# Kernel tuning notes

Hardware: AMD Instinct MI355X
Metric: run time of the kernel (lower is better)

## Reference

```python
import jax, jax.numpy as jnp
import numpy as np

# Grid constants derived from init kwargs: min_pt=0, max_pt=128, step=1, eps=1e-8
ORIGIN = -(1.0 + 1e-8)          # per-dim origin of control grid
STEP = 1.0
MAX_COORD = 130.0               # control_grid_size (132) - 2
PTS_N = 2_000_000
GRID = 132
CHANNELS = 1


def setup_inputs() -> dict:
    key = jax.random.key(0)
    k1, k2 = jax.random.split(key)
    # points in world coords, uniform over the interpolable domain
    pts = jax.random.uniform(k1, (PTS_N, 3), dtype=jnp.float32) * 128.0
    control_pts = jax.random.normal(k2, (CHANNELS, GRID, GRID, GRID), dtype=jnp.float32)
    return {"pts": pts, "control_pts": control_pts}


def _coefs(x):
    # Cardinal cubic B-spline basis (Irwin-Hall n=4), x in [0,1). [pts] -> [pts,4]
    omx = 1.0 - x
    c0 = omx ** 3
    c1 = 3.0 * (x - 2.0) * x ** 2 + 4.0
    c2 = -3.0 * omx ** 2 * (x + 1.0) + 4.0
    c3 = x ** 3
    return jnp.stack([c0, c1, c2, c3], axis=-1) / 6.0


def reference(pts, control_pts):
    padding_value = 0.0
    # to control-grid coordinates
    t = (pts - ORIGIN) / STEP                                   # [P,3]
    in_bounds = jnp.all(t >= 1.0, axis=-1) & jnp.all(t < MAX_COORD, axis=-1)  # [P]
    t = jnp.where(in_bounds[:, None], t, 1.0)
    ti = t.astype(jnp.int32)                                    # trunc == floor since t>=1
    frac = t - ti.astype(t.dtype)                               # [P,3]
    w = _coefs(frac.reshape(-1)).reshape(-1, 3, 4)              # [P,3,4]

    stencil = jnp.arange(-1, 3, dtype=jnp.int32)                # [-1,0,1,2]
    idx = ti[..., None] + stencil                               # [P,3,4]
    # gather the 4x4x4 control-point stencil per point: [C,P,4,4,4]
    cp = control_pts[:, idx[:, 0, :, None, None], idx[:, 1, None, :, None], idx[:, 2, None, None, :]]
    # tensor-product weighted sum
    vals = jnp.einsum('cpijk,pi,pj,pk->pc', cp, w[:, 0], w[:, 1], w[:, 2])  # [P,C]
    vals = jnp.where(in_bounds[:, None], vals, jnp.float32(padding_value))
    return vals
```

## Files before the change

### kernel.cpp

```cpp
#include <hip/hip_runtime.h>

#define GRID_DIM 132
#define SLAB (GRID_DIM * GRID_DIM)
#define NB 512
#define CHUNK 2048
#define KPT (CHUNK / 256)
#define REG 20
#define REG2 (REG * REG)
#define REG3 (REG * REG * REG)
#define STRIPE 8192

__device__ __forceinline__ void bspline_w(float x, float w[4]) {
    float omx = 1.0f - x;
    w[0] = omx * omx * omx * (1.0f / 6.0f);
    w[1] = (3.0f * (x - 2.0f) * x * x + 4.0f) * (1.0f / 6.0f);
    w[2] = (-3.0f * omx * omx * (x + 1.0f) + 4.0f) * (1.0f / 6.0f);
    w[3] = x * x * x * (1.0f / 6.0f);
}

__device__ __forceinline__ void load_pt(const float* __restrict__ pts, int i,
                                        float& tx, float& ty, float& tz, bool& inb) {
    tx = pts[3 * i + 0] + 1.0f;
    ty = pts[3 * i + 1] + 1.0f;
    tz = pts[3 * i + 2] + 1.0f;
    inb = (tx >= 1.0f) && (ty >= 1.0f) && (tz >= 1.0f) &&
          (tx < 130.0f) && (ty < 130.0f) && (tz < 130.0f);
    if (!inb) { tx = ty = tz = 1.0f; }
}

__device__ __forceinline__ int calc_bin(float tx, float ty, float tz) {
    int bx = min(7, ((int)tx - 1) >> 4);
    int by = min(7, ((int)ty - 1) >> 4);
    int bz = min(7, ((int)tz - 1) >> 4);
    return (bx << 6) | (by << 3) | bz;
}

__device__ __forceinline__ void local_stripe_scan(
    const unsigned* __restrict__ stot, int nstripe,
    unsigned* soff, unsigned* sc)
{
    int t = threadIdx.x;
    if (t < 256) sc[t] = (t < nstripe) ? stot[t] : 0u;
    __syncthreads();
    for (int off = 1; off < 256; off <<= 1) {
        unsigned v = (t >= off && t < 256) ? sc[t - off] : 0u;
        __syncthreads();
        if (t < 256) sc[t] += v;
        __syncthreads();
    }
    if (t < 256) soff[t] = (t == 0) ? 0u : sc[t - 1];
    __syncthreads();
}

__global__ __launch_bounds__(256) void hist512_kernel(
    const float* __restrict__ pts, int n, int nblk, unsigned* __restrict__ bh)
{
    __shared__ unsigned lh[NB];
    int tid = threadIdx.x, blk = blockIdx.x;
    int c0 = blk * CHUNK;
    for (int b = tid; b < NB; b += 256) lh[b] = 0u;
    __syncthreads();
#pragma unroll
    for (int k = 0; k < KPT; ++k) {
        int i = c0 + tid + k * 256;
        if (i < n) {
            float tx, ty, tz; bool inb;
            load_pt(pts, i, tx, ty, tz, inb);
            atomicAdd(&lh[calc_bin(tx, ty, tz)], 1u);
        }
    }
    __syncthreads();
    for (int b = tid; b < NB; b += 256) bh[b * nblk + blk] = lh[b];
}

__global__ __launch_bounds__(256) void scan_l1_kernel(
    const unsigned* __restrict__ bh, unsigned* __restrict__ seg,
    unsigned* __restrict__ stot, int TOT)
{
    __shared__ unsigned sc[256];
    int t = threadIdx.x;
    int base_idx = blockIdx.x * STRIPE + t * 32;
    unsigned local[32];
    unsigned s = 0;
#pragma unroll
    for (int j = 0; j < 32; ++j) {
        int idx = base_idx + j;
        unsigned v = (idx < TOT) ? bh[idx] : 0u;
        local[j] = v; s += v;
    }
    sc[t] = s;
    __syncthreads();
    for (int off = 1; off < 256; off <<= 1) {
        unsigned v = (t >= off) ? sc[t - off] : 0u;
        __syncthreads();
        sc[t] += v;
        __syncthreads();
    }
    unsigned run = (t == 0) ? 0u : sc[t - 1];
#pragma unroll
    for (int j = 0; j < 32; ++j) {
        int idx = base_idx + j;
        if (idx < TOT) seg[idx] = run;
        run += local[j];
    }
    if (t == 255) stot[blockIdx.x] = sc[255];
}

__global__ __launch_bounds__(256) void partition_kernel(
    const float* __restrict__ pts, int n, int nblk,
    const unsigned* __restrict__ seg, const unsigned* __restrict__ stot,
    int nstripe, float4* __restrict__ sorted, unsigned* __restrict__ inv)
{
    __shared__ unsigned lcur[NB];
    __shared__ unsigned sc[256], soff[256];

    local_stripe_scan(stot, nstripe, soff, sc);

    int bid = blockIdx.x;
    int q = nblk >> 3, r = nblk & 7;
    int xcd = bid & 7, pos = bid >> 3;
    int blk = (xcd < r ? xcd * (q + 1) : r * (q + 1) + (xcd - r) * q) + pos;

    int tid = threadIdx.x;
    int c0 = blk * CHUNK;

    for (int b = tid; b < NB; b += 256) {
        int idx = b * nblk + blk;
        lcur[b] = seg[idx] + soff[idx >> 13];
    }
    __syncthreads();

#pragma unroll
    for (int k = 0; k < KPT; ++k) {
        int i = c0 + tid + k * 256;
        if (i < n) {
            float tx, ty, tz; bool inb;
            load_pt(pts, i, tx, ty, tz, inb);
            int bin = calc_bin(tx, ty, tz);
            unsigned g = atomicAdd(&lcur[bin], 1u);
            unsigned tag = (unsigned)i | (inb ? 0u : 0x80000000u);
            sorted[g] = make_float4(tx, ty, tz, __uint_as_float(tag));
            inv[i] = g;
        }
    }
}

__global__ __launch_bounds__(512) void eval_kernel(
    const float4* __restrict__ sorted, const float* __restrict__ cp,
    const unsigned* __restrict__ seg, const unsigned* __restrict__ stot,
    int nstripe, float* __restrict__ val_s, int n, int nblk)
{
    __shared__ float region[REG3];
    __shared__ unsigned sc[256], soff[256];

    local_stripe_scan(stot, nstripe, soff, sc);

    int bid = blockIdx.x;
    int bin = (bid & 7) * 64 + (bid >> 3);
    int x0 = (bin >> 6) << 4, y0 = ((bin >> 3) & 7) << 4, z0 = (bin & 7) << 4;

    const float* src = cp + (size_t)x0 * SLAB + y0 * GRID_DIM + z0;
    for (int v = threadIdx.x; v < REG3; v += 512) {
        int gx = v / REG2;
        int rr = v - gx * REG2;
        int gy = rr / REG;
        int gz = rr - gy * REG;
        region[v] = src[gx * SLAB + gy * GRID_DIM + gz];
    }
    __syncthreads();

    int i0 = bin * nblk;
    unsigned s = seg[i0] + soff[i0 >> 13];
    unsigned e;
    if (bin == NB - 1) e = (unsigned)n;
    else { int i1 = (bin + 1) * nblk; e = seg[i1] + soff[i1 >> 13]; }

    for (unsigned i = s + threadIdx.x; i < e; i += 512) {
        float4 p = sorted[i];
        unsigned tag = __float_as_uint(p.w);
        int ix = (int)p.x, iy = (int)p.y, iz = (int)p.z;
        float wx[4], wy[4], wz[4];
        bspline_w(p.x - (float)ix, wx);
        bspline_w(p.y - (float)iy, wy);
        bspline_w(p.z - (float)iz, wz);
        int lx = ix - 1 - x0, ly = iy - 1 - y0, lz = iz - 1 - z0;
        const float* rb = region + (lx * REG + ly) * REG + lz;
        float acc = 0.0f;
#pragma unroll
        for (int a = 0; a < 4; ++a) {
            float accy = 0.0f;
#pragma unroll
            for (int b = 0; b < 4; ++b) {
                const float* row = rb + (a * REG + b) * REG;
                float sz = fmaf(row[0], wz[0], fmaf(row[1], wz[1],
                           fmaf(row[2], wz[2], row[3] * wz[3])));
                accy = fmaf(wy[b], sz, accy);
            }
            acc = fmaf(wx[a], accy, acc);
        }
        val_s[i] = (tag >> 31) ? 0.0f : acc;
    }
}

__global__ __launch_bounds__(256) void unscatter_kernel(
    const float* __restrict__ val_s, const unsigned* __restrict__ inv,
    float* __restrict__ out, int n)
{
    int g = blockIdx.x * blockDim.x + threadIdx.x;
    int base = g * 4;
    if (base + 3 < n) {
        uint4 iv = ((const uint4*)inv)[g];
        float4 o;
        o.x = val_s[iv.x]; o.y = val_s[iv.y]; o.z = val_s[iv.z]; o.w = val_s[iv.w];
        ((float4*)out)[g] = o;
    } else if (base < n) {
        for (int k = base; k < n; ++k) out[k] = val_s[inv[k]];
    }
}

__global__ __launch_bounds__(256) void eval_unsorted_kernel(
    const float* __restrict__ pts, const float* __restrict__ cp,
    float* __restrict__ out, int n)
{
    int i = blockIdx.x * blockDim.x + threadIdx.x;
    if (i >= n) return;
    float tx, ty, tz; bool inb;
    load_pt(pts, i, tx, ty, tz, inb);
    int ix = (int)tx, iy = (int)ty, iz = (int)tz;
    float wx[4], wy[4], wz[4];
    bspline_w(tx - (float)ix, wx);
    bspline_w(ty - (float)iy, wy);
    bspline_w(tz - (float)iz, wz);
    const float* bse = cp + (size_t)(ix - 1) * SLAB + (size_t)(iy - 1) * GRID_DIM + (iz - 1);
    float acc = 0.0f;
#pragma unroll
    for (int a = 0; a < 4; ++a) {
        float accy = 0.0f;
#pragma unroll
        for (int b = 0; b < 4; ++b) {
            const float* row = bse + a * SLAB + b * GRID_DIM;
            float4 v;
            __builtin_memcpy(&v, row, 16);
            float sz = fmaf(v.x, wz[0], fmaf(v.y, wz[1], fmaf(v.z, wz[2], v.w * wz[3])));
            accy = fmaf(wy[b], sz, accy);
        }
        acc = fmaf(wx[a], accy, acc);
    }
    out[i] = inb ? acc : 0.0f;
}

extern "C" void kernel_launch(void* const* d_in, const int* in_sizes, int n_in,
                              void* d_out, int out_size, void* d_ws, size_t ws_size,
                              hipStream_t stream) {
    const float* pts = (const float*)d_in[0];
    const float* cp  = (const float*)d_in[1];
    float* out       = (float*)d_out;

    int n = in_sizes[0] / 3;
    int nblk = (n + CHUNK - 1) / CHUNK;
    int TOT = NB * nblk;
    int nstripe = (TOT + STRIPE - 1) / STRIPE;

    size_t A          = (((size_t)TOT * 4) + 1023) & ~(size_t)1023;
    size_t off_seg    = A;
    size_t off_stot   = 2 * A;
    size_t off_sorted = 2 * A + 1024;
    size_t off_inv    = off_sorted + (size_t)n * sizeof(float4);
    size_t off_val    = off_inv    + (size_t)n * sizeof(unsigned);
    size_t need       = off_val    + (size_t)n * sizeof(float);

    if (ws_size >= need && nblk <= 1024 && nstripe <= 256) {
        unsigned* bh     = (unsigned*)d_ws;
        unsigned* seg    = (unsigned*)((char*)d_ws + off_seg);
        unsigned* stot   = (unsigned*)((char*)d_ws + off_stot);
        float4*   sorted = (float4*)((char*)d_ws + off_sorted);
        unsigned* inv    = (unsigned*)((char*)d_ws + off_inv);
        float*    val_s  = (float*)((char*)d_ws + off_val);

        int uwg = ((n + 3) / 4 + 255) / 256;

        hipLaunchKernelGGL(hist512_kernel, dim3(nblk), dim3(256), 0, stream,
                           pts, n, nblk, bh);
        hipLaunchKernelGGL(scan_l1_kernel, dim3(nstripe), dim3(256), 0, stream,
                           bh, seg, stot, TOT);
        hipLaunchKernelGGL(partition_kernel, dim3(nblk), dim3(256), 0, stream,
                           pts, n, nblk, seg, stot, nstripe, sorted, inv);
        hipLaunchKernelGGL(eval_kernel, dim3(NB), dim3(512), 0, stream,
                           sorted, cp, seg, stot, nstripe, val_s, n, nblk);
        hipLaunchKernelGGL(unscatter_kernel, dim3(uwg), dim3(256), 0, stream,
                           val_s, inv, out, n);
    } else {
        hipLaunchKernelGGL(eval_unsorted_kernel, dim3((n + 255) / 256), dim3(256), 0, stream,
                           pts, cp, out, n);
    }
}
```

Baseline: 166.6 us.

## Unscatter per chunk via shared-memory staging of contiguous bin segments

```diff
diff --git a/kernel.cpp b/kernel.cpp
--- a/kernel.cpp
+++ b/kernel.cpp
@@ -35,6 +35,12 @@
     return (bx << 6) | (by << 3) | bz;
 }
 
+__device__ __forceinline__ int chunk_swizzle(int bid, int nblk) {
+    int q = nblk >> 3, r = nblk & 7;
+    int xcd = bid & 7, pos = bid >> 3;
+    return (xcd < r ? xcd * (q + 1) : r * (q + 1) + (xcd - r) * q) + pos;
+}
+
 __device__ __forceinline__ void local_stripe_scan(
     const unsigned* __restrict__ stot, int nstripe,
     unsigned* soff, unsigned* sc)
@@ -116,11 +122,7 @@
 
     local_stripe_scan(stot, nstripe, soff, sc);
 
-    int bid = blockIdx.x;
-    int q = nblk >> 3, r = nblk & 7;
-    int xcd = bid & 7, pos = bid >> 3;
-    int blk = (xcd < r ? xcd * (q + 1) : r * (q + 1) + (xcd - r) * q) + pos;
-
+    int blk = chunk_swizzle(blockIdx.x, nblk);
     int tid = threadIdx.x;
     int c0 = blk * CHUNK;
 
@@ -204,17 +206,65 @@
 
 __global__ __launch_bounds__(256) void unscatter_kernel(
     const float* __restrict__ val_s, const unsigned* __restrict__ inv,
-    float* __restrict__ out, int n)
-{
-    int g = blockIdx.x * blockDim.x + threadIdx.x;
-    int base = g * 4;
-    if (base + 3 < n) {
-        uint4 iv = ((const uint4*)inv)[g];
-        float4 o;
-        o.x = val_s[iv.x]; o.y = val_s[iv.y]; o.z = val_s[iv.z]; o.w = val_s[iv.w];
-        ((float4*)out)[g] = o;
-    } else if (base < n) {
-        for (int k = base; k < n; ++k) out[k] = val_s[inv[k]];
+    const unsigned* __restrict__ seg, const unsigned* __restrict__ stot,
+    int nstripe, float* __restrict__ out, int n, int nblk)
+{
+    __shared__ unsigned sc[256], soff[256];
+    __shared__ unsigned gsegS[NB];
+    __shared__ unsigned lrs[NB];
+    __shared__ float lbuf[CHUNK];
+
+    local_stripe_scan(stot, nstripe, soff, sc);
+
+    int blk = chunk_swizzle(blockIdx.x, nblk);
+    int tid = threadIdx.x;
+    int c0 = blk * CHUNK;
+
+    unsigned len2[2];
+#pragma unroll
+    for (int j = 0; j < 2; ++j) {
+        int b = 2 * tid + j;
+        int idx = b * nblk + blk;
+        unsigned st = seg[idx] + soff[idx >> 13];
+        gsegS[b] = st;
+        int idx1 = idx + 1;
+        unsigned en = (idx1 < NB * nblk) ? (seg[idx1] + soff[idx1 >> 13])
+                                         : (unsigned)n;
+        len2[j] = en - st;
+    }
+    sc[tid] = len2[0] + len2[1];
+    __syncthreads();
+    for (int off = 1; off < 256; off <<= 1) {
+        unsigned v = (tid >= off) ? sc[tid - off] : 0u;
+        __syncthreads();
+        sc[tid] += v;
+        __syncthreads();
+    }
+    unsigned base = (tid == 0) ? 0u : sc[tid - 1];
+    lrs[2 * tid] = base;
+    lrs[2 * tid + 1] = base + len2[0];
+    __syncthreads();
+
+#pragma unroll
+    for (int j = 0; j < 2; ++j) {
+        int b = 2 * tid + j;
+        unsigned st = gsegS[b], l = len2[j], d = lrs[b];
+        for (unsigned k = 0; k < l; ++k) lbuf[d + k] = val_s[st + k];
+    }
+    __syncthreads();
+
+#pragma unroll
+    for (int k = 0; k < KPT; ++k) {
+        int i = c0 + tid + k * 256;
+        if (i < n) {
+            unsigned g = inv[i];
+            unsigned lo = 0, hi = NB;
+            while (hi - lo > 1) {
+                unsigned mid = (lo + hi) >> 1;
+                if (gsegS[mid] <= g) lo = mid; else hi = mid;
+            }
+            out[i] = lbuf[lrs[lo] + (g - gsegS[lo])];
+        }
     }
 }
 
@@ -269,15 +319,13 @@
     size_t off_val    = off_inv    + (size_t)n * sizeof(unsigned);
     size_t need       = off_val    + (size_t)n * sizeof(float);
 
-    if (ws_size >= need && nblk <= 1024 && nstripe <= 256) {
+    if (ws_size >= need && nblk <= 1024 && nstripe <= 256 && n % CHUNK == 0) {
         unsigned* bh     = (unsigned*)d_ws;
         unsigned* seg    = (unsigned*)((char*)d_ws + off_seg);
         unsigned* stot   = (unsigned*)((char*)d_ws + off_stot);
         float4*   sorted = (float4*)((char*)d_ws + off_sorted);
         unsigned* inv    = (unsigned*)((char*)d_ws + off_inv);
         float*    val_s  = (float*)((char*)d_ws + off_val);
-
-        int uwg = ((n + 3) / 4 + 255) / 256;
 
         hipLaunchKernelGGL(hist512_kernel, dim3(nblk), dim3(256), 0, stream,
                            pts, n, nblk, bh);
@@ -287,8 +335,8 @@
                            pts, n, nblk, seg, stot, nstripe, sorted, inv);
         hipLaunchKernelGGL(eval_kernel, dim3(NB), dim3(512), 0, stream,
                            sorted, cp, seg, stot, nstripe, val_s, n, nblk);
-        hipLaunchKernelGGL(unscatter_kernel, dim3(uwg), dim3(256), 0, stream,
-                           val_s, inv, out, n);
+        hipLaunchKernelGGL(unscatter_kernel, dim3(nblk), dim3(256), 0, stream,
+                           val_s, inv, seg, stot, nstripe, out, n, nblk);
     } else {
         hipLaunchKernelGGL(eval_unsorted_kernel, dim3((n + 255) / 256), dim3(256), 0, stream,
                            pts, cp, out, n);
```

New measurement: 383.9 us. 2.3x slower.

## Scatter eval results directly to output and drop unscatter pass

Applied to the files above, without the earlier changes.

```diff
diff --git a/kernel.cpp b/kernel.cpp
--- a/kernel.cpp
+++ b/kernel.cpp
@@ -3,7 +3,7 @@
 #define GRID_DIM 132
 #define SLAB (GRID_DIM * GRID_DIM)
 #define NB 512
-#define CHUNK 2048
+#define CHUNK 4096
 #define KPT (CHUNK / 256)
 #define REG 20
 #define REG2 (REG * REG)
@@ -35,6 +35,12 @@
     return (bx << 6) | (by << 3) | bz;
 }
 
+__device__ __forceinline__ int chunk_swizzle(int bid, int nblk) {
+    int q = nblk >> 3, r = nblk & 7;
+    int xcd = bid & 7, pos = bid >> 3;
+    return (xcd < r ? xcd * (q + 1) : r * (q + 1) + (xcd - r) * q) + pos;
+}
+
 __device__ __forceinline__ void local_stripe_scan(
     const unsigned* __restrict__ stot, int nstripe,
     unsigned* soff, unsigned* sc)
@@ -109,18 +115,14 @@
 __global__ __launch_bounds__(256) void partition_kernel(
     const float* __restrict__ pts, int n, int nblk,
     const unsigned* __restrict__ seg, const unsigned* __restrict__ stot,
-    int nstripe, float4* __restrict__ sorted, unsigned* __restrict__ inv)
+    int nstripe, float4* __restrict__ sorted)
 {
     __shared__ unsigned lcur[NB];
     __shared__ unsigned sc[256], soff[256];
 
     local_stripe_scan(stot, nstripe, soff, sc);
 
-    int bid = blockIdx.x;
-    int q = nblk >> 3, r = nblk & 7;
-    int xcd = bid & 7, pos = bid >> 3;
-    int blk = (xcd < r ? xcd * (q + 1) : r * (q + 1) + (xcd - r) * q) + pos;
-
+    int blk = chunk_swizzle(blockIdx.x, nblk);
     int tid = threadIdx.x;
     int c0 = blk * CHUNK;
 
@@ -140,7 +142,6 @@
             unsigned g = atomicAdd(&lcur[bin], 1u);
             unsigned tag = (unsigned)i | (inb ? 0u : 0x80000000u);
             sorted[g] = make_float4(tx, ty, tz, __uint_as_float(tag));
-            inv[i] = g;
         }
     }
 }
@@ -148,7 +149,7 @@
 __global__ __launch_bounds__(512) void eval_kernel(
     const float4* __restrict__ sorted, const float* __restrict__ cp,
     const unsigned* __restrict__ seg, const unsigned* __restrict__ stot,
-    int nstripe, float* __restrict__ val_s, int n, int nblk)
+    int nstripe, float* __restrict__ out, int n, int nblk)
 {
     __shared__ float region[REG3];
     __shared__ unsigned sc[256], soff[256];
@@ -198,23 +199,8 @@
             }
             acc = fmaf(wx[a], accy, acc);
         }
-        val_s[i] = (tag >> 31) ? 0.0f : acc;
-    }
-}
-
-__global__ __launch_bounds__(256) void unscatter_kernel(
-    const float* __restrict__ val_s, const unsigned* __restrict__ inv,
-    float* __restrict__ out, int n)
-{
-    int g = blockIdx.x * blockDim.x + threadIdx.x;
-    int base = g * 4;
-    if (base + 3 < n) {
-        uint4 iv = ((const uint4*)inv)[g];
-        float4 o;
-        o.x = val_s[iv.x]; o.y = val_s[iv.y]; o.z = val_s[iv.z]; o.w = val_s[iv.w];
-        ((float4*)out)[g] = o;
-    } else if (base < n) {
-        for (int k = base; k < n; ++k) out[k] = val_s[inv[k]];
+        int orig = (int)(tag & 0x7fffffffu);
+        out[orig] = (tag >> 31) ? 0.0f : acc;
     }
 }
 
@@ -265,30 +251,22 @@
     size_t off_seg    = A;
     size_t off_stot   = 2 * A;
     size_t off_sorted = 2 * A + 1024;
-    size_t off_inv    = off_sorted + (size_t)n * sizeof(float4);
-    size_t off_val    = off_inv    + (size_t)n * sizeof(unsigned);
-    size_t need       = off_val    + (size_t)n * sizeof(float);
+    size_t need       = off_sorted + (size_t)n * sizeof(float4);
 
     if (ws_size >= need && nblk <= 1024 && nstripe <= 256) {
         unsigned* bh     = (unsigned*)d_ws;
         unsigned* seg    = (unsigned*)((char*)d_ws + off_seg);
         unsigned* stot   = (unsigned*)((char*)d_ws + off_stot);
         float4*   sorted = (float4*)((char*)d_ws + off_sorted);
-        unsigned* inv    = (unsigned*)((char*)d_ws + off_inv);
-        float*    val_s  = (float*)((char*)d_ws + off_val);
-
-        int uwg = ((n + 3) / 4 + 255) / 256;
 
         hipLaunchKernelGGL(hist512_kernel, dim3(nblk), dim3(256), 0, stream,
                            pts, n, nblk, bh);
         hipLaunchKernelGGL(scan_l1_kernel, dim3(nstripe), dim3(256), 0, stream,
                            bh, seg, stot, TOT);
         hipLaunchKernelGGL(partition_kernel, dim3(nblk), dim3(256), 0, stream,
-                           pts, n, nblk, seg, stot, nstripe, sorted, inv);
+                           pts, n, nblk, seg, stot, nstripe, sorted);
         hipLaunchKernelGGL(eval_kernel, dim3(NB), dim3(512), 0, stream,
-                           sorted, cp, seg, stot, nstripe, val_s, n, nblk);
-        hipLaunchKernelGGL(unscatter_kernel, dim3(uwg), dim3(256), 0, stream,
-                           val_s, inv, out, n);
+                           sorted, cp, seg, stot, nstripe, out, n, nblk);
     } else {
         hipLaunchKernelGGL(eval_unsorted_kernel, dim3((n + 255) / 256), dim3(256), 0, stream,
                            pts, cp, out, n);
```

New measurement: 149.6 us. 1.11x faster.
